# Kernel tuning notes

Hardware: AMD Instinct MI355X
Metric: run time of the kernel (lower is better)

## Reference

```python
import jax, jax.numpy as jnp
import numpy as np

CA, CZ, CS, CSI = 128, 128, 384, 256
NH, HD, NB, A = 8, 16, 6, 7
RMAX, SMAX = 32, 2
RELP_DIM = 4 * (RMAX + 1) + 1 + 2 * (SMAX + 1)  # 139


def make_relp(L):
    # single-chain relative-position features: [L, L, 139]
    i = jnp.arange(L)
    d = i[:, None] - i[None, :]
    a_rel_pos = jax.nn.one_hot(jnp.clip(d + RMAX, 0, 2 * RMAX), 2 * (RMAX + 1))
    d_tok = jnp.where(d == 0, RMAX, 2 * RMAX + 1)  # same-res only on diagonal
    a_rel_tok = jax.nn.one_hot(d_tok, 2 * (RMAX + 1))
    same_ent = jnp.ones((L, L, 1), jnp.float32)
    a_rel_chain = jax.nn.one_hot(jnp.full((L, L), SMAX), 2 * (SMAX + 1))
    return jnp.concatenate([a_rel_pos, a_rel_tok, same_ent, a_rel_chain], axis=-1)


def ln(x, g, b):
    m = x.mean(-1, keepdims=True)
    v = ((x - m) ** 2).mean(-1, keepdims=True)
    return (x - m) / jnp.sqrt(v + 1e-5) * g + b


def setup_inputs():
    key = jax.random.key(0)
    ks = iter(jax.random.split(key, 64))
    def p(*shape):
        return (jax.random.normal(next(ks), shape, jnp.float32) * 0.05)
    B, Ns, L = 1, 2, 384
    inp = dict(
        x_t=jax.random.normal(next(ks), (B, Ns, L, A, 3), jnp.float32),
        sigma=jax.random.uniform(next(ks), (B, Ns), jnp.float32),
        s_inputs=jax.random.normal(next(ks), (B, L, CSI), jnp.float32),
        s_trunk=jax.random.normal(next(ks), (B, L, CS), jnp.float32),
        z_trunk=jax.random.normal(next(ks), (B, L, L, CZ), jnp.float32),
        token_mask=jnp.ones((B, L), bool),
        s_in_w=p(CSI, CS), s_in_b=p(CS),
        relp_w=p(RELP_DIM, CZ), relp_b=p(CZ),
        t1_w=p(1, CS), t1_b=p(CS), t2_w=p(CS, CS), t2_b=p(CS),
        xp_w=p(3 * A, CA), xp_b=p(CA),
        s2a_w=p(CS, CA), s2a_b=p(CA),
        out_w=p(CA, 3 * A), out_b=p(3 * A),
        an_g=jnp.ones((NB, CA)), an_b=jnp.zeros((NB, CA)),
        zn_g=jnp.ones((NB, CZ)), zn_b=jnp.zeros((NB, CZ)),
        qw=p(NB, CA, CA), qb=p(NB, CA),
        kw=p(NB, CA, CA), kb=p(NB, CA),
        vw=p(NB, CA, CA), vb=p(NB, CA),
        zw=p(NB, CZ, NH), zb=p(NB, NH),
        ow=p(NB, CA, CA), ob=p(NB, CA),
        f1w=p(NB, CA, 4 * CA), f1b=p(NB, 4 * CA),
        f2w=p(NB, 4 * CA, CA), f2b=p(NB, CA),
    )
    return inp


def reference(x_t, sigma, s_inputs, s_trunk, z_trunk, token_mask,
              s_in_w, s_in_b, relp_w, relp_b, t1_w, t1_b, t2_w, t2_b,
              xp_w, xp_b, s2a_w, s2a_b, out_w, out_b,
              an_g, an_b, zn_g, zn_b, qw, qb, kw, kb, vw, vb,
              zw, zb, ow, ob, f1w, f1b, f2w, f2b):
    B, Ns, L = x_t.shape[:3]
    relp = make_relp(L)                                   # [L, L, 139]
    pair_z = z_trunk + relp @ relp_w + relp_b             # [B, L, L, CZ]
    s_cond = s_trunk + s_inputs @ s_in_w + s_in_b         # [B, L, CS]
    t_feat = jax.nn.silu(sigma.reshape(B * Ns, 1) @ t1_w + t1_b) @ t2_w + t2_b
    single_s = s_cond[:, None] + t_feat.reshape(B, Ns, CS)[:, :, None]  # [B,Ns,L,CS]
    a = x_t.reshape(B, Ns, L, 3 * A) @ xp_w + xp_b + single_s @ s2a_w + s2a_b
    a2 = a.reshape(B * Ns, L, CA)
    z2 = jnp.broadcast_to(pair_z[:, None], (B, Ns, L, L, CZ)).reshape(B * Ns, L, L, CZ)
    m = jnp.broadcast_to(token_mask[:, None], (B, Ns, L)).reshape(B * Ns, L)
    pair_mask = m[:, :, None] & m[:, None, :]             # [B*Ns, L, L]
    scale = 1.0 / np.sqrt(HD).astype(np.float32)
    for i in range(NB):
        an = ln(a2, an_g[i], an_b[i])
        zn = ln(z2, zn_g[i], zn_b[i])
        q = (an @ qw[i] + qb[i]).reshape(-1, L, NH, HD)
        k = (an @ kw[i] + kb[i]).reshape(-1, L, NH, HD)
        v = (an @ vw[i] + vb[i]).reshape(-1, L, NH, HD)
        logits = jnp.einsum('blhd,bmhd->bhlm', q, k) * scale
        bias = (zn @ zw[i] + zb[i]).transpose(0, 3, 1, 2)  # [B*Ns, NH, L, L]
        logits = jnp.where(pair_mask[:, None], logits + bias, -1e9)
        attn = jax.nn.softmax(logits, axis=-1)
        o = jnp.einsum('bhlm,bmhd->blhd', attn, v).reshape(-1, L, CA)
        a2 = a2 + (o @ ow[i] + ob[i])
        an2 = ln(a2, an_g[i], an_b[i])
        a2 = a2 + jax.nn.gelu(an2 @ f1w[i] + f1b[i], approximate=False) @ f2w[i] + f2b[i]
    vout = (a2 @ out_w + out_b).reshape(B, Ns, L, A, 3)
    return vout * token_mask[:, None, :, None, None].astype(vout.dtype)
```

## Files before the change

kernel.cpp:

```cpp
#include <hip/hip_runtime.h>
#include <math.h>

#define L 384
#define CA 128
#define NH 8
#define HD 16
#define NB 6
#define NS 2
#define NP (L*L)

typedef __attribute__((ext_vector_type(4))) float f32x4;
typedef __attribute__((ext_vector_type(8))) short s16x8;
typedef __attribute__((ext_vector_type(4))) unsigned short u16x4;
typedef unsigned short ushort_t;

__device__ inline unsigned short f2bf(float f){
  union { float f; unsigned int u; } v; v.f = f;
  unsigned int u = v.u;
  unsigned int r = u + 0x7FFF + ((u>>16)&1);
  return (unsigned short)(r>>16);
}
__device__ inline float bf2f(ushort_t u){
  union { float f; unsigned int i; } v; v.i = ((unsigned int)u)<<16; return v.f;
}

__global__ __launch_bounds__(384) void k0_setup(
    const float* sigma, const float* t1w, const float* t1b,
    const float* t2w, const float* t2b,
    const float* zng, const float* znb, const float* zw, const float* zb,
    float* t_feat, float* wz, float* cb){
  int b = blockIdx.x, t = threadIdx.x;
  if(b==0){
    __shared__ float sil[2][384];
    for(int s=0;s<2;s++){
      float x = sigma[s]*t1w[t] + t1b[t];
      sil[s][t] = x / (1.f + expf(-x));
    }
    __syncthreads();
    for(int s=0;s<2;s++){
      float acc = t2b[t];
      for(int k=0;k<384;k++) acc += sil[s][k]*t2w[k*384+t];
      t_feat[s*384+t] = acc;
    }
  } else if(b==1){
    for(int idx=t; idx<128*48; idx+=384){
      int c = idx/48, o = idx%48, blk=o>>3, h=o&7;
      wz[idx] = zng[blk*128+c]*zw[(blk*128+c)*8+h];
    }
  } else {
    if(t<48){
      int blk=t>>3, h=t&7;
      float acc = zb[blk*8+h];
      for(int c=0;c<128;c++) acc += znb[blk*128+c]*zw[(blk*128+c)*8+h];
      cb[t] = acc;
    }
  }
}

#define WT_LAYER 196608
__global__ __launch_bounds__(256) void k_prep(
    const float* qw, const float* kw, const float* vw,
    const float* f1w, const float* f2w, const float* ow,
    const float* wz, const float* relp_w, const float* relp_b,
    const float* s_in_w, const float* s2a_w,
    ushort_t* wT, ushort_t* wzT, float* rbase,
    ushort_t* s_in_wT, ushort_t* s2a_wT){
  int b = blockIdx.x, t = threadIdx.x;
  if(b == 324){
    for(int idx=t; idx<6144; idx+=256){
      int h = idx>>7, c = idx&127;
      wzT[h*128+c] = f2bf(wz[c*48+h]);
    }
    if(t<128) rbase[t] = relp_w[132*128+t] + relp_w[135*128+t] + relp_b[t];
    return;
  }
  __shared__ float tl[64][65];
  const float* src; ushort_t* dst;
  int M, N, k0, n0;
  if(b < 96){
    int mat = b>>2, li = mat>>2, wsel = mat&3, tile = b&3;
    const float* const ws_[4] = {qw, kw, vw, ow};
    const int off_[4] = {0, 16384, 32768, 180224};
    src = ws_[wsel] + (size_t)li*16384;
    dst = wT + (size_t)li*WT_LAYER + off_[wsel];
    M = 128; N = 128; k0 = (tile>>1)*64; n0 = (tile&1)*64;
  } else if(b < 192){
    int idx = b-96, li = idx>>4, tile = idx&15;
    src = f1w + (size_t)li*65536;
    dst = wT + (size_t)li*WT_LAYER + 49152;
    M = 128; N = 512; k0 = (tile>>3)*64; n0 = (tile&7)*64;
  } else if(b < 288){
    int idx = b-192, li = idx>>4, tile = idx&15;
    src = f2w + (size_t)li*65536;
    dst = wT + (size_t)li*WT_LAYER + 114688;
    M = 512; N = 128; k0 = (tile>>1)*64; n0 = (tile&1)*64;
  } else if(b < 312){
    int tile = b-288;
    src = s_in_w; dst = s_in_wT;
    M = 256; N = 384; k0 = (tile/6)*64; n0 = (tile%6)*64;
  } else {
    int tile = b-312;
    src = s2a_w; dst = s2a_wT;
    M = 384; N = 128; k0 = (tile>>1)*64; n0 = (tile&1)*64;
  }
  for(int i=t;i<4096;i+=256){
    int r=i>>6, c=i&63;
    tl[r][c] = src[(size_t)(k0+r)*N + n0+c];
  }
  __syncthreads();
  for(int i=t;i<4096;i+=256){
    int r=i>>6, c=i&63;
    dst[(size_t)(n0+r)*M + k0+c] = f2bf(tl[c][r]);
  }
}

__global__ __launch_bounds__(256) void k2_bias(
    const float* z_trunk, const float* relp_w, const float* rbase,
    const ushort_t* wzT, const float* cb, ushort_t* bias_all){
  __shared__ float lds_c[48][65];
  int t = threadIdx.x, lane = t&63, wv = t>>6;
  int rowf = lane&15, kg = lane>>4;
  int p = blockIdx.x*64 + wv*16 + rowf;
  int i = p/L, j = p - i*L, d = i - j;
  int r1 = d+32; r1 = r1<0?0:(r1>64?64:r1);
  int r2 = (d==0) ? 98 : 131;
  const float* zp  = z_trunk + (size_t)p*128;
  const float* w1p = relp_w + r1*128;
  const float* w2p = relp_w + r2*128;

  float val[4][8];
  float s = 0.f;
  #pragma unroll
  for(int ks=0; ks<4; ks++){
    int c0 = ks*32 + kg*8;
    f32x4 za = *(const f32x4*)(zp +c0), zb2 = *(const f32x4*)(zp +c0+4);
    f32x4 wa = *(const f32x4*)(w1p+c0), wb = *(const f32x4*)(w1p+c0+4);
    f32x4 ua = *(const f32x4*)(w2p+c0), ub = *(const f32x4*)(w2p+c0+4);
    f32x4 ra = *(const f32x4*)(rbase+c0), rb = *(const f32x4*)(rbase+c0+4);
    #pragma unroll
    for(int jj=0;jj<4;jj++){
      val[ks][jj]   = za[jj]+wa[jj]+ua[jj]+ra[jj];
      val[ks][jj+4] = zb2[jj]+wb[jj]+ub[jj]+rb[jj];
      s += val[ks][jj] + val[ks][jj+4];
    }
  }
  s += __shfl_xor(s,16,64); s += __shfl_xor(s,32,64);
  float mean = s*(1.f/128.f);
  float q2 = 0.f;
  #pragma unroll
  for(int ks=0; ks<4; ks++)
    #pragma unroll
    for(int jj=0;jj<8;jj++){ float dd = val[ks][jj]-mean; q2 += dd*dd; }
  q2 += __shfl_xor(q2,16,64); q2 += __shfl_xor(q2,32,64);
  float rstd = rsqrtf(q2*(1.f/128.f) + 1e-5f);

  s16x8 af[4];
  #pragma unroll
  for(int ks=0; ks<4; ks++)
    #pragma unroll
    for(int jj=0;jj<8;jj++) af[ks][jj] = (short)f2bf((val[ks][jj]-mean)*rstd);

  #pragma unroll
  for(int ht=0; ht<3; ht++){
    int col = ht*16 + rowf;
    float cbv = cb[col];
    f32x4 acc = {cbv,cbv,cbv,cbv};
    #pragma unroll
    for(int ks=0; ks<4; ks++){
      s16x8 bf = *(const s16x8*)&wzT[col*128 + ks*32 + kg*8];
      acc = __builtin_amdgcn_mfma_f32_16x16x32_bf16(af[ks], bf, acc, 0,0,0);
    }
    #pragma unroll
    for(int i2=0;i2<4;i2++) lds_c[col][wv*16 + kg*4 + i2] = acc[i2];
  }
  __syncthreads();
  int p0 = blockIdx.x*64;
  for(int idx=t; idx<3072; idx+=256){
    int h = idx>>6, c = idx&63;
    bias_all[(size_t)h*NP + p0 + c] = f2bf(lds_c[h][c]);
  }
}

__device__ inline void qkv_project(ushort_t zh[16][152], const ushort_t* wTl,
                                   const float* qb, const float* kb, const float* vb,
                                   ushort_t* q_bf, ushort_t* k_bf, ushort_t* vT_bf,
                                   int s_idx, int lbase, int wv, int rowf, int kg){
  s16x8 af[4];
  #pragma unroll
  for(int ks=0;ks<4;ks++) af[ks] = *(const s16x8*)&zh[rowf][ks*32 + kg*8];
  #pragma unroll
  for(int u=0;u<6;u++){
    int unit = wv*6 + u;
    int proj = unit>>3, nt = unit&7;
    int col = nt*16 + rowf;
    const ushort_t* wp = wTl + proj*16384;
    const float* bias = proj==0? qb : (proj==1? kb : vb);
    float bv = bias[col];
    f32x4 acc = {bv,bv,bv,bv};
    #pragma unroll
    for(int ks=0;ks<4;ks++){
      s16x8 bf = *(const s16x8*)&wp[col*128 + ks*32 + kg*8];
      acc = __builtin_amdgcn_mfma_f32_16x16x32_bf16(af[ks], bf, acc, 0,0,0);
    }
    int sh = s_idx*NH + nt;
    if(proj==2){
      #pragma unroll
      for(int i2=0;i2<4;i2++)
        vT_bf[((size_t)sh*16 + rowf)*384 + lbase + kg*4 + i2] = f2bf(acc[i2]);
    } else {
      float sc = (proj==0)? 0.25f : 1.0f;
      ushort_t* outp = (proj==0)? q_bf : k_bf;
      #pragma unroll
      for(int i2=0;i2<4;i2++)
        outp[((size_t)sh*384 + lbase + kg*4 + i2)*16 + rowf] = f2bf(acc[i2]*sc);
    }
  }
}

__global__ __launch_bounds__(256) void k_qkv0(
    const float* x_t, const float* s_inputs, const float* s_trunk,
    const float* s_in_b, const ushort_t* s_in_wT,
    const float* s2a_b, const ushort_t* s2a_wT,
    const float* xp_w, const float* xp_b, const float* t_feat,
    const float* g, const float* bb,
    const ushort_t* wTl, const float* qb, const float* kb, const float* vb,
    float* a2, ushort_t* q_bf, ushort_t* k_bf, ushort_t* vT_bf){
  __shared__ ushort_t si[16][280];
  __shared__ ushort_t scb[16][408];
  __shared__ float xrow[16][21];
  __shared__ float a_new[16][132];
  __shared__ ushort_t zh[16][152];
  int t = threadIdx.x, lane = t&63, wv = t>>6;
  int rowf = lane&15, kg = lane>>4;
  int bid = blockIdx.x, s_idx = bid/24, lt = bid%24;
  int lr0 = lt*16;

  for(int i=t;i<16*256;i+=256){
    int r=i>>8, c=i&255;
    si[r][c] = f2bf(s_inputs[(size_t)(lr0+r)*256+c]);
  }
  for(int i=t;i<16*21;i+=256){
    int r=i/21, u=i%21;
    xrow[r][u] = x_t[((size_t)s_idx*L + lr0 + r)*21 + u];
  }
  __syncthreads();

  {
    s16x8 af1[8];
    #pragma unroll
    for(int ks=0;ks<8;ks++) af1[ks] = *(const s16x8*)&si[rowf][ks*32+kg*8];
    const float* tf = t_feat + s_idx*384;
    #pragma unroll
    for(int nn=0;nn<6;nn++){
      int col = (wv*6+nn)*16 + rowf;
      float bv = s_in_b[col];
      f32x4 acc = {bv,bv,bv,bv};
      #pragma unroll
      for(int ks=0;ks<8;ks++){
        s16x8 bf = *(const s16x8*)&s_in_wT[col*256 + ks*32 + kg*8];
        acc = __builtin_amdgcn_mfma_f32_16x16x32_bf16(af1[ks], bf, acc, 0,0,0);
      }
      float tfc = tf[col];
      #pragma unroll
      for(int i2=0;i2<4;i2++){
        int r = kg*4+i2;
        scb[r][col] = f2bf(acc[i2] + s_trunk[(size_t)(lr0+r)*384+col] + tfc);
      }
    }
  }
  __syncthreads();

  {
    s16x8 xf[12];
    #pragma unroll
    for(int ks=0;ks<12;ks++) xf[ks] = *(const s16x8*)&scb[rowf][ks*32+kg*8];
    #pragma unroll
    for(int nn=0;nn<2;nn++){
      int col = (wv*2+nn)*16 + rowf;
      float base = xp_b[col] + s2a_b[col];
      f32x4 acc;
      #pragma unroll
      for(int i2=0;i2<4;i2++){
        float xc = base;
        #pragma unroll
        for(int u=0;u<21;u++) xc += xrow[kg*4+i2][u]*xp_w[u*128+col];
        acc[i2] = xc;
      }
      #pragma unroll
      for(int ks=0;ks<12;ks++){
        s16x8 bf = *(const s16x8*)&s2a_wT[col*384 + ks*32 + kg*8];
        acc = __builtin_amdgcn_mfma_f32_16x16x32_bf16(xf[ks], bf, acc, 0,0,0);
      }
      #pragma unroll
      for(int i2=0;i2<4;i2++){
        int r = kg*4+i2;
        a_new[r][col] = acc[i2];
        a2[((size_t)(s_idx*L + lr0 + r))*128 + col] = acc[i2];
      }
    }
  }
  __syncthreads();

  {
    int row = t>>4, sub = t&15;
    const float* xp = &a_new[row][sub*8];
    f32x4 x0 = *(const f32x4*)xp;
    f32x4 x1 = *(const f32x4*)(xp+4);
    float s = x0[0]+x0[1]+x0[2]+x0[3]+x1[0]+x1[1]+x1[2]+x1[3];
    s += __shfl_xor(s,1,64); s += __shfl_xor(s,2,64);
    s += __shfl_xor(s,4,64); s += __shfl_xor(s,8,64);
    float mean = s*(1.f/128.f);
    float q2 = 0.f;
    #pragma unroll
    for(int jj=0;jj<4;jj++){ float d0=x0[jj]-mean, d1=x1[jj]-mean; q2 += d0*d0+d1*d1; }
    q2 += __shfl_xor(q2,1,64); q2 += __shfl_xor(q2,2,64);
    q2 += __shfl_xor(q2,4,64); q2 += __shfl_xor(q2,8,64);
    float rstd = rsqrtf(q2*(1.f/128.f)+1e-5f);
    int c0 = sub*8;
    f32x4 g0 = *(const f32x4*)(g+c0), g1 = *(const f32x4*)(g+c0+4);
    f32x4 b0 = *(const f32x4*)(bb+c0), b1 = *(const f32x4*)(bb+c0+4);
    s16x8 pack;
    #pragma unroll
    for(int jj=0;jj<4;jj++){
      pack[jj]   = (short)f2bf((x0[jj]-mean)*rstd*g0[jj]+b0[jj]);
      pack[jj+4] = (short)f2bf((x1[jj]-mean)*rstd*g1[jj]+b1[jj]);
    }
    *(s16x8*)&zh[row][c0] = pack;
  }
  __syncthreads();
  qkv_project(zh, wTl, qb, kb, vb, q_bf, k_bf, vT_bf, s_idx, lr0, wv, rowf, kg);
}

__global__ __launch_bounds__(1024) void k_fused(
    float* a2, const float* an_g, const float* an_b, const ushort_t* wT,
    const float* qb_all, const float* kb_all, const float* vb_all,
    const float* ob_all, const float* f1b_all, const float* f2b_all,
    ushort_t* q_bf, ushort_t* k_bf, ushort_t* vT_bf,
    const ushort_t* bias_all, const float* out_w, const float* out_b,
    float* out, int li){
  __shared__ ushort_t P_lds[16][16][88];
  __shared__ float orow[16][132];
  __shared__ float a_new[16][132];
  __shared__ ushort_t zh[16][152];
  __shared__ ushort_t h_lds[16][536];
  __shared__ float ocomb[8][16][20];
  __shared__ float lcomb[8][16];
  __shared__ float fcomb[8][16][20];

  int t = threadIdx.x, lane = t&63, wv = t>>6;
  int rowf = lane&15, kg = lane>>4;
  int bid = blockIdx.x, s_idx = bid/24, qt = bid%24;
  int r0 = bid*16;
  const ushort_t* wTl = wT + (size_t)li*WT_LAYER;
  const float* g  = an_g + li*128;
  const float* bb = an_b + li*128;

  {
    int h = wv>>1, kh = wv&1;
    int sh = s_idx*NH + h;
    ushort_t (*Pw)[88] = P_lds[wv];
    s16x8 qf = {0,0,0,0,0,0,0,0};
    if(kg < 2) qf = *(const s16x8*)&q_bf[((size_t)sh*384 + qt*16 + rowf)*16 + kg*8];
    const ushort_t* kp = k_bf + (size_t)sh*384*16;
    const ushort_t* vp = vT_bf + ((size_t)sh*16 + rowf)*384;
    const ushort_t* bbp = bias_all + (size_t)li*8*NP + (size_t)h*NP
                        + (size_t)(qt*16 + rowf)*L;

    f32x4 o0 = {0,0,0,0}, o1 = {0,0,0,0};
    float l_acc = 0.f;
    for(int c=0;c<3;c++){
      int key0 = kh*192 + c*64;
      f32x4 st[4];
      #pragma unroll
      for(int t4=0;t4<4;t4++){
        s16x8 kf = {0,0,0,0,0,0,0,0};
        if(kg < 2) kf = *(const s16x8*)&kp[((size_t)(key0 + t4*16 + rowf))*16 + kg*8];
        u16x4 bb4 = *(const u16x4*)&bbp[key0 + t4*16 + kg*4];
        f32x4 cin;
        #pragma unroll
        for(int jj=0;jj<4;jj++) cin[jj] = bf2f(bb4[jj]);
        st[t4] = __builtin_amdgcn_mfma_f32_16x16x32_bf16(kf, qf, cin, 0,0,0);
      }
      #pragma unroll
      for(int t4=0;t4<4;t4++){
        float p0 = __expf(st[t4][0]), p1 = __expf(st[t4][1]);
        float p2 = __expf(st[t4][2]), p3 = __expf(st[t4][3]);
        l_acc += (p0+p1)+(p2+p3);
        u16x4 pk = {f2bf(p0), f2bf(p1), f2bf(p2), f2bf(p3)};
        *(u16x4*)&Pw[rowf][t4*16 + kg*4] = pk;
      }
      {
        s16x8 pa = *(const s16x8*)&Pw[rowf][kg*8];
        s16x8 vbf = *(const s16x8*)&vp[key0 + kg*8];
        o0 = __builtin_amdgcn_mfma_f32_16x16x32_bf16(pa, vbf, o0, 0,0,0);
        s16x8 pb = *(const s16x8*)&Pw[rowf][32 + kg*8];
        s16x8 vbf2 = *(const s16x8*)&vp[key0 + 32 + kg*8];
        o1 = __builtin_amdgcn_mfma_f32_16x16x32_bf16(pb, vbf2, o1, 0,0,0);
      }
    }
    f32x4 o_acc = o0 + o1;
    l_acc += __shfl_xor(l_acc, 16, 64);
    l_acc += __shfl_xor(l_acc, 32, 64);
    if(kh==1){
      #pragma unroll
      for(int i2=0;i2<4;i2++) ocomb[h][kg*4+i2][rowf] = o_acc[i2];
      if(kg==0) lcomb[h][rowf] = l_acc;
    }
    __syncthreads();
    if(kh==0){
      l_acc += lcomb[h][rowf];
      #pragma unroll
      for(int i2=0;i2<4;i2++) o_acc[i2] += ocomb[h][kg*4+i2][rowf];
      float inv = 1.f / l_acc;
      #pragma unroll
      for(int i2=0;i2<4;i2++){
        float invq = __shfl(inv, kg*4 + i2, 64);
        orow[kg*4+i2][h*16 + rowf] = o_acc[i2]*invq;
      }
    }
  }
  __syncthreads();

  if(wv < 8){
    s16x8 af[4];
    #pragma unroll
    for(int ks=0;ks<4;ks++){
      f32x4 v0 = *(const f32x4*)&orow[rowf][ks*32+kg*8];
      f32x4 v1 = *(const f32x4*)&orow[rowf][ks*32+kg*8+4];
      s16x8 p;
      #pragma unroll
      for(int jj=0;jj<4;jj++){ p[jj] = (short)f2bf(v0[jj]); p[jj+4] = (short)f2bf(v1[jj]); }
      af[ks] = p;
    }
    const ushort_t* wo = wTl + 180224;
    const float* obp = ob_all + li*128;
    int col = wv*16 + rowf;
    float bv = obp[col];
    f32x4 acc = {bv,bv,bv,bv};
    f32x4 accB = {0,0,0,0};
    #pragma unroll
    for(int ks=0;ks<2;ks++){
      s16x8 bf = *(const s16x8*)&wo[col*128 + ks*32 + kg*8];
      acc = __builtin_amdgcn_mfma_f32_16x16x32_bf16(af[ks], bf, acc, 0,0,0);
      s16x8 bf2 = *(const s16x8*)&wo[col*128 + (ks+2)*32 + kg*8];
      accB = __builtin_amdgcn_mfma_f32_16x16x32_bf16(af[ks+2], bf2, accB, 0,0,0);
    }
    acc += accB;
    #pragma unroll
    for(int i2=0;i2<4;i2++){
      int r = kg*4+i2;
      a_new[r][col] = a2[(size_t)(r0+r)*128 + col] + acc[i2];
    }
  }
  __syncthreads();

  {
    int row = wv, c0 = lane*2;
    float x0 = a_new[row][c0], x1 = a_new[row][c0+1];
    float s = x0+x1;
    s += __shfl_xor(s,1,64); s += __shfl_xor(s,2,64); s += __shfl_xor(s,4,64);
    s += __shfl_xor(s,8,64); s += __shfl_xor(s,16,64); s += __shfl_xor(s,32,64);
    float mean = s*(1.f/128.f);
    float d0=x0-mean, d1=x1-mean;
    float q2 = d0*d0+d1*d1;
    q2 += __shfl_xor(q2,1,64); q2 += __shfl_xor(q2,2,64); q2 += __shfl_xor(q2,4,64);
    q2 += __shfl_xor(q2,8,64); q2 += __shfl_xor(q2,16,64); q2 += __shfl_xor(q2,32,64);
    float rstd = rsqrtf(q2*(1.f/128.f)+1e-5f);
    unsigned int pk = (unsigned int)f2bf(d0*rstd*g[c0]+bb[c0])
                    | ((unsigned int)f2bf(d1*rstd*g[c0+1]+bb[c0+1])<<16);
    *(unsigned int*)&zh[row][c0] = pk;
  }
  __syncthreads();

  {
    s16x8 xf[4];
    #pragma unroll
    for(int ks=0;ks<4;ks++) xf[ks] = *(const s16x8*)&zh[rowf][ks*32 + kg*8];
    const ushort_t* w1 = wTl + 49152;
    const float* f1bp = f1b_all + li*512;
    #pragma unroll
    for(int nn=0; nn<2; nn++){
      int col = (wv*2+nn)*16 + rowf;
      float bv = f1bp[col];
      f32x4 acc = {bv,bv,bv,bv};
      #pragma unroll
      for(int ks=0;ks<4;ks++){
        s16x8 bf = *(const s16x8*)&w1[col*128 + ks*32 + kg*8];
        acc = __builtin_amdgcn_mfma_f32_16x16x32_bf16(xf[ks], bf, acc, 0,0,0);
      }
      #pragma unroll
      for(int i2=0;i2<4;i2++){
        float x = acc[i2];
        float ge = 0.5f*x*(1.f + erff(x*0.70710678f));
        h_lds[kg*4+i2][col] = f2bf(ge);
      }
    }
  }
  __syncthreads();

  {
    const ushort_t* w2 = wTl + 114688;
    const float* f2bp = f2b_all + li*128;
    int ct = wv>>1, kh2 = wv&1;
    int col2 = ct*16 + rowf;
    float bv = kh2? 0.f : f2bp[col2];
    f32x4 accA = {bv,bv,bv,bv};
    f32x4 accB = {0,0,0,0};
    int ks0 = kh2*8;
    #pragma unroll
    for(int kk=0; kk<4; kk++){
      s16x8 hfA = *(const s16x8*)&h_lds[rowf][(ks0+kk)*32 + kg*8];
      s16x8 bfA = *(const s16x8*)&w2[col2*512 + (ks0+kk)*32 + kg*8];
      accA = __builtin_amdgcn_mfma_f32_16x16x32_bf16(hfA, bfA, accA, 0,0,0);
      s16x8 hfB = *(const s16x8*)&h_lds[rowf][(ks0+kk+4)*32 + kg*8];
      s16x8 bfB = *(const s16x8*)&w2[col2*512 + (ks0+kk+4)*32 + kg*8];
      accB = __builtin_amdgcn_mfma_f32_16x16x32_bf16(hfB, bfB, accB, 0,0,0);
    }
    accA += accB;
    if(kh2==1){
      #pragma unroll
      for(int i2=0;i2<4;i2++) fcomb[ct][kg*4+i2][rowf] = accA[i2];
    }
    __syncthreads();
    if(kh2==0){
      #pragma unroll
      for(int i2=0;i2<4;i2++){
        int r = kg*4+i2;
        float fin = a_new[r][col2] + accA[i2] + fcomb[ct][r][rowf];
        a2[(size_t)(r0+r)*128 + col2] = fin;
        a_new[r][col2] = fin;
      }
    }
  }
  __syncthreads();

  if(li < NB-1){
    const float* g2  = an_g + (li+1)*128;
    const float* bb2 = an_b + (li+1)*128;
    {
      int row = wv, c0 = lane*2;
      float x0 = a_new[row][c0], x1 = a_new[row][c0+1];
      float s = x0+x1;
      s += __shfl_xor(s,1,64); s += __shfl_xor(s,2,64); s += __shfl_xor(s,4,64);
      s += __shfl_xor(s,8,64); s += __shfl_xor(s,16,64); s += __shfl_xor(s,32,64);
      float mean = s*(1.f/128.f);
      float d0=x0-mean, d1=x1-mean;
      float q2 = d0*d0+d1*d1;
      q2 += __shfl_xor(q2,1,64); q2 += __shfl_xor(q2,2,64); q2 += __shfl_xor(q2,4,64);
      q2 += __shfl_xor(q2,8,64); q2 += __shfl_xor(q2,16,64); q2 += __shfl_xor(q2,32,64);
      float rstd = rsqrtf(q2*(1.f/128.f)+1e-5f);
      unsigned int pk = (unsigned int)f2bf(d0*rstd*g2[c0]+bb2[c0])
                      | ((unsigned int)f2bf(d1*rstd*g2[c0+1]+bb2[c0+1])<<16);
      *(unsigned int*)&zh[row][c0] = pk;
    }
    __syncthreads();
    {
      const ushort_t* wTn = wT + (size_t)(li+1)*WT_LAYER;
      const float* qb2 = qb_all + (li+1)*128;
      const float* kb2 = kb_all + (li+1)*128;
      const float* vb2 = vb_all + (li+1)*128;
      s16x8 af[4];
      #pragma unroll
      for(int ks=0;ks<4;ks++) af[ks] = *(const s16x8*)&zh[rowf][ks*32 + kg*8];
      #pragma unroll
      for(int u=0;u<2;u++){
        int unit = wv + u*16;
        if(unit < 24){
          int proj = unit>>3, nt = unit&7;
          int col = nt*16 + rowf;
          const ushort_t* wp = wTn + proj*16384;
          const float* bias = proj==0? qb2 : (proj==1? kb2 : vb2);
          float bv = bias[col];
          f32x4 acc = {bv,bv,bv,bv};
          #pragma unroll
          for(int ks=0;ks<4;ks++){
            s16x8 bf = *(const s16x8*)&wp[col*128 + ks*32 + kg*8];
            acc = __builtin_amdgcn_mfma_f32_16x16x32_bf16(af[ks], bf, acc, 0,0,0);
          }
          int sh = s_idx*NH + nt;
          if(proj==2){
            #pragma unroll
            for(int i2=0;i2<4;i2++)
              vT_bf[((size_t)sh*16 + rowf)*384 + qt*16 + kg*4 + i2] = f2bf(acc[i2]);
          } else {
            float sc = (proj==0)? 0.25f : 1.0f;
            ushort_t* outp = (proj==0)? q_bf : k_bf;
            #pragma unroll
            for(int i2=0;i2<4;i2++)
              outp[((size_t)sh*384 + qt*16 + kg*4 + i2)*16 + rowf] = f2bf(acc[i2]*sc);
          }
        }
      }
    }
  } else {
    for(int idx=t; idx<336; idx+=1024){
      int r = idx/21, c = idx%21;
      float acc = out_b[c];
      #pragma unroll 8
      for(int kk=0;kk<128;kk++) acc += a_new[r][kk]*out_w[kk*21+c];
      out[(size_t)(r0+r)*21 + c] = acc;
    }
  }
}

extern "C" void kernel_launch(void* const* d_in, const int* in_sizes, int n_in,
                              void* d_out, int out_size, void* d_ws, size_t ws_size,
                              hipStream_t stream){
  const float* x_t      = (const float*)d_in[0];
  const float* sigma    = (const float*)d_in[1];
  const float* s_inputs = (const float*)d_in[2];
  const float* s_trunk  = (const float*)d_in[3];
  const float* z_trunk  = (const float*)d_in[4];
  const float* s_in_w = (const float*)d_in[6];
  const float* s_in_b = (const float*)d_in[7];
  const float* relp_w = (const float*)d_in[8];
  const float* relp_b = (const float*)d_in[9];
  const float* t1_w = (const float*)d_in[10];
  const float* t1_b = (const float*)d_in[11];
  const float* t2_w = (const float*)d_in[12];
  const float* t2_b = (const float*)d_in[13];
  const float* xp_w = (const float*)d_in[14];
  const float* xp_b = (const float*)d_in[15];
  const float* s2a_w = (const float*)d_in[16];
  const float* s2a_b = (const float*)d_in[17];
  const float* out_w = (const float*)d_in[18];
  const float* out_b = (const float*)d_in[19];
  const float* an_g = (const float*)d_in[20];
  const float* an_b = (const float*)d_in[21];
  const float* zn_g = (const float*)d_in[22];
  const float* zn_b = (const float*)d_in[23];
  const float* qw = (const float*)d_in[24];
  const float* qb = (const float*)d_in[25];
  const float* kw = (const float*)d_in[26];
  const float* kb = (const float*)d_in[27];
  const float* vw = (const float*)d_in[28];
  const float* vb = (const float*)d_in[29];
  const float* zw = (const float*)d_in[30];
  const float* zb = (const float*)d_in[31];
  const float* ow = (const float*)d_in[32];
  const float* ob = (const float*)d_in[33];
  const float* f1w = (const float*)d_in[34];
  const float* f1b = (const float*)d_in[35];
  const float* f2w = (const float*)d_in[36];
  const float* f2b = (const float*)d_in[37];

  float* ws = (float*)d_ws;
  ushort_t* bias_all = (ushort_t*)ws;
  float* wz     = ws + (size_t)24*NP;
  float* cb     = wz + 6144;
  float* t_feat = cb + 48;
  float* a2     = t_feat + 768;
  float* rbase  = a2 + (size_t)NS*L*CA;
  ushort_t* wT      = (ushort_t*)(rbase + 128);
  ushort_t* wzT     = wT + (size_t)6*WT_LAYER;
  ushort_t* q_bf    = wzT + 6144;
  ushort_t* k_bf    = q_bf + 98304;
  ushort_t* vT_bf   = k_bf + 98304;
  ushort_t* s_in_wT = vT_bf + 98304;
  ushort_t* s2a_wT  = s_in_wT + 98304;
  float* outp = (float*)d_out;

  k0_setup<<<3,384,0,stream>>>(sigma,t1_w,t1_b,t2_w,t2_b,zn_g,zn_b,zw,zb,t_feat,wz,cb);
  k_prep<<<325,256,0,stream>>>(qw,kw,vw,f1w,f2w,ow,wz,relp_w,relp_b,s_in_w,s2a_w,
                               wT,wzT,rbase,s_in_wT,s2a_wT);
  k2_bias<<<NP/64,256,0,stream>>>(z_trunk,relp_w,rbase,wzT,cb,bias_all);

  k_qkv0<<<48,256,0,stream>>>(x_t,s_inputs,s_trunk,s_in_b,s_in_wT,
                              s2a_b,s2a_wT,xp_w,xp_b,t_feat,
                              an_g, an_b, wT, qb, kb, vb,
                              a2, q_bf, k_bf, vT_bf);
  for(int i=0;i<NB;i++){
    k_fused<<<48,1024,0,stream>>>(a2, an_g, an_b, wT,
        qb, kb, vb, ob, f1b, f2b,
        q_bf, k_bf, vT_bf, bias_all,
        out_w, out_b, outp, i);
  }
}
```

Before: 242.8 us.

## Tile-major pair-bias layout staged through LDS; fold setup kernel into prep

The k2_bias kernel now writes the bf16 pair bias in a per-(layer, query-tile, head) contiguous layout. Each k_fused block bulk-loads its 8x16x384 bias tile into LDS with wide coalesced loads, instead of issuing scattered 8-byte global reads inside the attention loop. LDS is reused through a union between the attention-phase buffers and the post-attention buffers. The separate k0_setup kernel is merged into k_prep as extra blocks, removing one launch and the wz intermediate. The cost is a larger LDS footprint per block and an extra barrier before attention starts.

```diff
diff --git a/kernel.cpp b/kernel.cpp
--- a/kernel.cpp
+++ b/kernel.cpp
@@ -24,54 +24,46 @@
   union { float f; unsigned int i; } v; v.i = ((unsigned int)u)<<16; return v.f;
 }
 
-__global__ __launch_bounds__(384) void k0_setup(
-    const float* sigma, const float* t1w, const float* t1b,
-    const float* t2w, const float* t2b,
-    const float* zng, const float* znb, const float* zw, const float* zb,
-    float* t_feat, float* wz, float* cb){
-  int b = blockIdx.x, t = threadIdx.x;
-  if(b==0){
-    __shared__ float sil[2][384];
-    for(int s=0;s<2;s++){
-      float x = sigma[s]*t1w[t] + t1b[t];
-      sil[s][t] = x / (1.f + expf(-x));
-    }
-    __syncthreads();
-    for(int s=0;s<2;s++){
-      float acc = t2b[t];
-      for(int k=0;k<384;k++) acc += sil[s][k]*t2w[k*384+t];
-      t_feat[s*384+t] = acc;
-    }
-  } else if(b==1){
-    for(int idx=t; idx<128*48; idx+=384){
-      int c = idx/48, o = idx%48, blk=o>>3, h=o&7;
-      wz[idx] = zng[blk*128+c]*zw[(blk*128+c)*8+h];
-    }
-  } else {
-    if(t<48){
-      int blk=t>>3, h=t&7;
-      float acc = zb[blk*8+h];
-      for(int c=0;c<128;c++) acc += znb[blk*128+c]*zw[(blk*128+c)*8+h];
-      cb[t] = acc;
-    }
-  }
-}
-
 #define WT_LAYER 196608
 __global__ __launch_bounds__(256) void k_prep(
     const float* qw, const float* kw, const float* vw,
     const float* f1w, const float* f2w, const float* ow,
-    const float* wz, const float* relp_w, const float* relp_b,
+    const float* relp_w, const float* relp_b,
     const float* s_in_w, const float* s2a_w,
-    ushort_t* wT, ushort_t* wzT, float* rbase,
+    const float* sigma, const float* t1w, const float* t1b,
+    const float* t2w, const float* t2b,
+    const float* zng, const float* znb, const float* zw, const float* zb,
+    ushort_t* wT, ushort_t* wzT, float* rbase, float* cb, float* t_feat,
     ushort_t* s_in_wT, ushort_t* s2a_wT){
   int b = blockIdx.x, t = threadIdx.x;
   if(b == 324){
     for(int idx=t; idx<6144; idx+=256){
       int h = idx>>7, c = idx&127;
-      wzT[h*128+c] = f2bf(wz[c*48+h]);
+      wzT[h*128+c] = f2bf(zng[(h>>3)*128+c]*zw[((h>>3)*128+c)*8+(h&7)]);
     }
     if(t<128) rbase[t] = relp_w[132*128+t] + relp_w[135*128+t] + relp_b[t];
+    if(t<48){
+      int blk=t>>3, hh=t&7;
+      float acc = zb[t];
+      for(int c=0;c<128;c++) acc += znb[blk*128+c]*zw[(blk*128+c)*8+hh];
+      cb[t] = acc;
+    }
+    return;
+  }
+  if(b == 325){
+    __shared__ float sil[2][384];
+    for(int i=t;i<768;i+=256){
+      int s=i/384, k=i%384;
+      float x = sigma[s]*t1w[k] + t1b[k];
+      sil[s][k] = x / (1.f + expf(-x));
+    }
+    __syncthreads();
+    for(int o=t;o<768;o+=256){
+      int s=o/384, c=o%384;
+      float acc = t2b[c];
+      for(int k=0;k<384;k++) acc += sil[s][k]*t2w[k*384+c];
+      t_feat[s*384+c] = acc;
+    }
     return;
   }
   __shared__ float tl[64][65];
@@ -175,9 +167,11 @@
   }
   __syncthreads();
   int p0 = blockIdx.x*64;
+  int i0 = p0/L, qt_ = i0>>4, q16 = i0&15, j0 = p0 - i0*L;
   for(int idx=t; idx<3072; idx+=256){
-    int h = idx>>6, c = idx&63;
-    bias_all[(size_t)h*NP + p0 + c] = f2bf(lds_c[h][c]);
+    int pl = idx>>6, c = idx&63;
+    int li_ = pl>>3, h_ = pl&7;
+    bias_all[(size_t)((li_*24+qt_)*8+h_)*6144 + q16*384 + j0 + c] = f2bf(lds_c[pl][c]);
   }
 }
 
@@ -338,14 +332,22 @@
     ushort_t* q_bf, ushort_t* k_bf, ushort_t* vT_bf,
     const ushort_t* bias_all, const float* out_w, const float* out_b,
     float* out, int li){
-  __shared__ ushort_t P_lds[16][16][88];
   __shared__ float orow[16][132];
-  __shared__ float a_new[16][132];
-  __shared__ ushort_t zh[16][152];
-  __shared__ ushort_t h_lds[16][536];
   __shared__ float ocomb[8][16][20];
   __shared__ float lcomb[8][16];
-  __shared__ float fcomb[8][16][20];
+  union SM {
+    struct {
+      ushort_t bias[8][16][392];
+      ushort_t P[16][16][72];
+    } fl;
+    struct {
+      float a_new[16][132];
+      ushort_t zh[16][152];
+      ushort_t h_lds[16][536];
+      float fcomb[8][16][20];
+    } post;
+  };
+  __shared__ SM sm;
 
   int t = threadIdx.x, lane = t&63, wv = t>>6;
   int rowf = lane&15, kg = lane>>4;
@@ -356,15 +358,25 @@
   const float* bb = an_b + li*128;
 
   {
+    const ushort_t* btile = bias_all + (size_t)(li*24+qt)*8*6144;
+    #pragma unroll
+    for(int it=0; it<6; it++){
+      int idx = t + it*1024;
+      int row2 = idx/48, seg = idx%48;
+      *(s16x8*)&sm.fl.bias[row2>>4][row2&15][seg*8] =
+          *(const s16x8*)&btile[(size_t)row2*384 + seg*8];
+    }
+  }
+  __syncthreads();
+
+  {
     int h = wv>>1, kh = wv&1;
     int sh = s_idx*NH + h;
-    ushort_t (*Pw)[88] = P_lds[wv];
+    ushort_t (*Pw)[72] = sm.fl.P[wv];
     s16x8 qf = {0,0,0,0,0,0,0,0};
     if(kg < 2) qf = *(const s16x8*)&q_bf[((size_t)sh*384 + qt*16 + rowf)*16 + kg*8];
     const ushort_t* kp = k_bf + (size_t)sh*384*16;
     const ushort_t* vp = vT_bf + ((size_t)sh*16 + rowf)*384;
-    const ushort_t* bbp = bias_all + (size_t)li*8*NP + (size_t)h*NP
-                        + (size_t)(qt*16 + rowf)*L;
 
     f32x4 o0 = {0,0,0,0}, o1 = {0,0,0,0};
     float l_acc = 0.f;
@@ -375,7 +387,7 @@
       for(int t4=0;t4<4;t4++){
         s16x8 kf = {0,0,0,0,0,0,0,0};
         if(kg < 2) kf = *(const s16x8*)&kp[((size_t)(key0 + t4*16 + rowf))*16 + kg*8];
-        u16x4 bb4 = *(const u16x4*)&bbp[key0 + t4*16 + kg*4];
+        u16x4 bb4 = *(const u16x4*)&sm.fl.bias[h][rowf][key0 + t4*16 + kg*4];
         f32x4 cin;
         #pragma unroll
         for(int jj=0;jj<4;jj++) cin[jj] = bf2f(bb4[jj]);
@@ -449,14 +461,14 @@
     #pragma unroll
     for(int i2=0;i2<4;i2++){
       int r = kg*4+i2;
-      a_new[r][col] = a2[(size_t)(r0+r)*128 + col] + acc[i2];
+      sm.post.a_new[r][col] = a2[(size_t)(r0+r)*128 + col] + acc[i2];
     }
   }
   __syncthreads();
 
   {
     int row = wv, c0 = lane*2;
-    float x0 = a_new[row][c0], x1 = a_new[row][c0+1];
+    float x0 = sm.post.a_new[row][c0], x1 = sm.post.a_new[row][c0+1];
     float s = x0+x1;
     s += __shfl_xor(s,1,64); s += __shfl_xor(s,2,64); s += __shfl_xor(s,4,64);
     s += __shfl_xor(s,8,64); s += __shfl_xor(s,16,64); s += __shfl_xor(s,32,64);
@@ -468,14 +480,14 @@
     float rstd = rsqrtf(q2*(1.f/128.f)+1e-5f);
     unsigned int pk = (unsigned int)f2bf(d0*rstd*g[c0]+bb[c0])
                     | ((unsigned int)f2bf(d1*rstd*g[c0+1]+bb[c0+1])<<16);
-    *(unsigned int*)&zh[row][c0] = pk;
+    *(unsigned int*)&sm.post.zh[row][c0] = pk;
   }
   __syncthreads();
 
   {
     s16x8 xf[4];
     #pragma unroll
-    for(int ks=0;ks<4;ks++) xf[ks] = *(const s16x8*)&zh[rowf][ks*32 + kg*8];
+    for(int ks=0;ks<4;ks++) xf[ks] = *(const s16x8*)&sm.post.zh[rowf][ks*32 + kg*8];
     const ushort_t* w1 = wTl + 49152;
     const float* f1bp = f1b_all + li*512;
     #pragma unroll
@@ -492,7 +504,7 @@
       for(int i2=0;i2<4;i2++){
         float x = acc[i2];
         float ge = 0.5f*x*(1.f + erff(x*0.70710678f));
-        h_lds[kg*4+i2][col] = f2bf(ge);
+        sm.post.h_lds[kg*4+i2][col] = f2bf(ge);
       }
     }
   }
@@ -509,26 +521,26 @@
     int ks0 = kh2*8;
     #pragma unroll
     for(int kk=0; kk<4; kk++){
-      s16x8 hfA = *(const s16x8*)&h_lds[rowf][(ks0+kk)*32 + kg*8];
+      s16x8 hfA = *(const s16x8*)&sm.post.h_lds[rowf][(ks0+kk)*32 + kg*8];
       s16x8 bfA = *(const s16x8*)&w2[col2*512 + (ks0+kk)*32 + kg*8];
       accA = __builtin_amdgcn_mfma_f32_16x16x32_bf16(hfA, bfA, accA, 0,0,0);
-      s16x8 hfB = *(const s16x8*)&h_lds[rowf][(ks0+kk+4)*32 + kg*8];
+      s16x8 hfB = *(const s16x8*)&sm.post.h_lds[rowf][(ks0+kk+4)*32 + kg*8];
       s16x8 bfB = *(const s16x8*)&w2[col2*512 + (ks0+kk+4)*32 + kg*8];
       accB = __builtin_amdgcn_mfma_f32_16x16x32_bf16(hfB, bfB, accB, 0,0,0);
     }
     accA += accB;
     if(kh2==1){
       #pragma unroll
-      for(int i2=0;i2<4;i2++) fcomb[ct][kg*4+i2][rowf] = accA[i2];
+      for(int i2=0;i2<4;i2++) sm.post.fcomb[ct][kg*4+i2][rowf] = accA[i2];
     }
     __syncthreads();
     if(kh2==0){
       #pragma unroll
       for(int i2=0;i2<4;i2++){
         int r = kg*4+i2;
-        float fin = a_new[r][col2] + accA[i2] + fcomb[ct][r][rowf];
+        float fin = sm.post.a_new[r][col2] + accA[i2] + sm.post.fcomb[ct][r][rowf];
         a2[(size_t)(r0+r)*128 + col2] = fin;
-        a_new[r][col2] = fin;
+        sm.post.a_new[r][col2] = fin;
       }
     }
   }
@@ -539,7 +551,7 @@
     const float* bb2 = an_b + (li+1)*128;
     {
       int row = wv, c0 = lane*2;
-      float x0 = a_new[row][c0], x1 = a_new[row][c0+1];
+      float x0 = sm.post.a_new[row][c0], x1 = sm.post.a_new[row][c0+1];
       float s = x0+x1;
       s += __shfl_xor(s,1,64); s += __shfl_xor(s,2,64); s += __shfl_xor(s,4,64);
       s += __shfl_xor(s,8,64); s += __shfl_xor(s,16,64); s += __shfl_xor(s,32,64);
@@ -551,7 +563,7 @@
       float rstd = rsqrtf(q2*(1.f/128.f)+1e-5f);
       unsigned int pk = (unsigned int)f2bf(d0*rstd*g2[c0]+bb2[c0])
                       | ((unsigned int)f2bf(d1*rstd*g2[c0+1]+bb2[c0+1])<<16);
-      *(unsigned int*)&zh[row][c0] = pk;
+      *(unsigned int*)&sm.post.zh[row][c0] = pk;
     }
     __syncthreads();
     {
@@ -561,7 +573,7 @@
       const float* vb2 = vb_all + (li+1)*128;
       s16x8 af[4];
       #pragma unroll
-      for(int ks=0;ks<4;ks++) af[ks] = *(const s16x8*)&zh[rowf][ks*32 + kg*8];
+      for(int ks=0;ks<4;ks++) af[ks] = *(const s16x8*)&sm.post.zh[rowf][ks*32 + kg*8];
       #pragma unroll
       for(int u=0;u<2;u++){
         int unit = wv + u*16;
@@ -597,7 +609,7 @@
       int r = idx/21, c = idx%21;
       float acc = out_b[c];
       #pragma unroll 8
-      for(int kk=0;kk<128;kk++) acc += a_new[r][kk]*out_w[kk*21+c];
+      for(int kk=0;kk<128;kk++) acc += sm.post.a_new[r][kk]*out_w[kk*21+c];
       out[(size_t)(r0+r)*21 + c] = acc;
     }
   }
@@ -646,8 +658,7 @@
 
   float* ws = (float*)d_ws;
   ushort_t* bias_all = (ushort_t*)ws;
-  float* wz     = ws + (size_t)24*NP;
-  float* cb     = wz + 6144;
+  float* cb     = ws + (size_t)24*NP;
   float* t_feat = cb + 48;
   float* a2     = t_feat + 768;
   float* rbase  = a2 + (size_t)NS*L*CA;
@@ -660,9 +671,9 @@
   ushort_t* s2a_wT  = s_in_wT + 98304;
   float* outp = (float*)d_out;
 
-  k0_setup<<<3,384,0,stream>>>(sigma,t1_w,t1_b,t2_w,t2_b,zn_g,zn_b,zw,zb,t_feat,wz,cb);
-  k_prep<<<325,256,0,stream>>>(qw,kw,vw,f1w,f2w,ow,wz,relp_w,relp_b,s_in_w,s2a_w,
-                               wT,wzT,rbase,s_in_wT,s2a_wT);
+  k_prep<<<326,256,0,stream>>>(qw,kw,vw,f1w,f2w,ow,relp_w,relp_b,s_in_w,s2a_w,
+                               sigma,t1_w,t1_b,t2_w,t2_b,zn_g,zn_b,zw,zb,
+                               wT,wzT,rbase,cb,t_feat,s_in_wT,s2a_wT);
   k2_bias<<<NP/64,256,0,stream>>>(z_trunk,relp_w,rbase,wzT,cb,bias_all);
 
   k_qkv0<<<48,256,0,stream>>>(x_t,s_inputs,s_trunk,s_in_b,s_in_wT,
```

Measured after the change: 233.9 us. 1.04x faster.
